# Kernel optimization log

Hardware: AMD Instinct MI355X
Metric: run time of the kernel (lower is better)

## Reference

```python
import jax, jax.numpy as jnp
from jax import lax
import numpy as np

NH = 4                      # num_heads in CrossScaleCom
KS = [3, 5, 7, 9]           # per-head depthwise kernel sizes
WS = 2                      # window_size in LocalFeatureGuided
GGM_K = 7                   # guide-token generator kernel size


def _dwconv(x, w, stride, pad):
    # depthwise conv: w has shape (C, 1, k, k), feature_group_count = C
    return lax.conv_general_dilated(
        x, w, (stride, stride), [(pad, pad), (pad, pad)],
        feature_group_count=x.shape[1],
        dimension_numbers=("NCHW", "OIHW", "NCHW"))


def _forward(x, dw_w0, dw_b0, dw_w1, dw_b1, dw_w2, dw_b2, dw_w3, dw_b3,
             csc_w, csc_b, bn_gamma, bn_beta, bn_mean, bn_var,
             ggm_w, ggm_b, qkv_w, qkv_b, proj_w, proj_b):
    B, C, H, W = x.shape
    cph = C // NH
    # ---- CrossScaleCom: per-head multi-scale depthwise convs ----
    xh = x.reshape(B, NH, cph, H, W)
    dws = [(dw_w0, dw_b0), (dw_w1, dw_b1), (dw_w2, dw_b2), (dw_w3, dw_b3)]
    heads = [_dwconv(xh[:, i], w, 1, KS[i] // 2) + b[None, :, None, None]
             for i, (w, b) in enumerate(dws)]
    y = jnp.stack(heads, 1)                      # (B, NH, cph, H, W)
    y = y.transpose(0, 2, 1, 3, 4).reshape(B, C, H, W)  # channel shuffle
    y = jnp.einsum("bchw,oc->bohw", y, csc_w) + csc_b[None, :, None, None]
    Co = y.shape[1]
    # ---- LocalFeatureGuided ----
    # ggm: BatchNorm (eval) -> GELU (exact) -> depthwise conv k=7 stride=WS
    inv = bn_gamma / jnp.sqrt(bn_var + 1e-5)
    g = (y - bn_mean[None, :, None, None]) * inv[None, :, None, None] \
        + bn_beta[None, :, None, None]
    g = jax.nn.gelu(g, approximate=False)
    g = _dwconv(g, ggm_w, WS, GGM_K // 2) + ggm_b[None, :, None, None]  # (B,Co,Ho,Wo)
    Ho, Wo = H // WS, W // WS
    L = Ho * Wo
    # unfold(kernel=WS, stride=WS) -> (B, Co, WS*WS, L), torch unfold ordering
    xu = y.reshape(B, Co, Ho, WS, Wo, WS).transpose(0, 1, 3, 5, 2, 4)
    xu = xu.reshape(B, Co, WS * WS, L)
    tokens = jnp.concatenate([g.reshape(B, Co, 1, L), xu], axis=2)  # (B,Co,5,L)
    # 1x1 conv over channel dim == einsum
    qkv = jnp.einsum("bcpl,oc->bopl", tokens, qkv_w) + qkv_b[None, :, None, None]
    q, k, v = jnp.split(qkv, 3, axis=1)          # each (B, Co, 5, L)
    # tiny 5x5 attention per (batch, channel), contracting over windows L
    attn = jnp.einsum("bcpl,bcql->bcpq", q, k) / (Co ** 0.5)
    attn = jax.nn.softmax(attn, axis=-1)
    out = jnp.einsum("bcpq,bcql->bcpl", attn, v)  # (B, Co, 5, L)
    out = out[:, :, 0, :].reshape(B, Co, Ho, Wo)  # guide-token output
    out = jnp.einsum("bchw,oc->bohw", out, proj_w) + proj_b[None, :, None, None]
    return out


def setup_inputs() -> dict:
    key = jax.random.key(0)
    ks = jax.random.split(key, 16)
    B, Cin, Cout, H, W = 8, 64, 128, 224, 224
    cph = Cin // NH
    s = 0.05
    d = {"x": jax.random.normal(ks[0], (B, Cin, H, W), jnp.float32)}
    for i, kk in enumerate(KS):
        d[f"dw_w{i}"] = jax.random.normal(ks[1 + i], (cph, 1, kk, kk), jnp.float32) * s
        d[f"dw_b{i}"] = jnp.zeros((cph,), jnp.float32)
    d["csc_w"] = jax.random.normal(ks[5], (Cout, Cin), jnp.float32) * s
    d["csc_b"] = jnp.zeros((Cout,), jnp.float32)
    d["bn_gamma"] = jnp.ones((Cout,), jnp.float32)
    d["bn_beta"] = jnp.zeros((Cout,), jnp.float32)
    d["bn_mean"] = jnp.zeros((Cout,), jnp.float32)
    d["bn_var"] = jnp.ones((Cout,), jnp.float32)
    d["ggm_w"] = jax.random.normal(ks[6], (Cout, 1, GGM_K, GGM_K), jnp.float32) * s
    d["ggm_b"] = jnp.zeros((Cout,), jnp.float32)
    d["qkv_w"] = jax.random.normal(ks[7], (3 * Cout, Cout), jnp.float32) * s
    d["qkv_b"] = jnp.zeros((3 * Cout,), jnp.float32)
    d["proj_w"] = jax.random.normal(ks[8], (Cout, Cout), jnp.float32) * s
    d["proj_b"] = jnp.zeros((Cout,), jnp.float32)
    return d


def reference(x, dw_w0, dw_b0, dw_w1, dw_b1, dw_w2, dw_b2, dw_w3, dw_b3,
              csc_w, csc_b, bn_gamma, bn_beta, bn_mean, bn_var,
              ggm_w, ggm_b, qkv_w, qkv_b, proj_w, proj_b):
    return _forward(x, dw_w0, dw_b0, dw_w1, dw_b1, dw_w2, dw_b2, dw_w3, dw_b3,
                    csc_w, csc_b, bn_gamma, bn_beta, bn_mean, bn_var,
                    ggm_w, ggm_b, qkv_w, qkv_b, proj_w, proj_b)
```

## Files before the change

### kernel.cpp

```cpp
#include <hip/hip_runtime.h>

#define BB 8
#define CIN 64
#define CO 128
#define Hdim 224
#define Wdim 224
#define HWt (224*224)
#define HO 112
#define WO 112
#define Lt (112*112)

typedef unsigned short u16;
typedef short bf16x8 __attribute__((ext_vector_type(8)));
typedef float f32x4  __attribute__((ext_vector_type(4)));
#define MFMA16(a,b,c) __builtin_amdgcn_mfma_f32_16x16x32_bf16((a),(b),(c),0,0,0)

__device__ inline u16 f2bf(float f) {
    union { float f; unsigned u; } v; v.f = f;
    unsigned r = (v.u + 0x7fffu + ((v.u >> 16) & 1u)) >> 16;
    return (u16)r;
}
__device__ inline float bf2f(u16 h) {
    union { unsigned u; float f; } v; v.u = ((unsigned)h) << 16; return v.f;
}
__device__ inline float sum8bf(uint4 v) {
    return bf2f(v.x & 0xffff) + bf2f(v.x >> 16) + bf2f(v.y & 0xffff) + bf2f(v.y >> 16)
         + bf2f(v.z & 0xffff) + bf2f(v.z >> 16) + bf2f(v.w & 0xffff) + bf2f(v.w >> 16);
}

__global__ void zero_kernel(float* __restrict__ p, int n4) {
    int i = blockIdx.x * 256 + threadIdx.x;
    if (i < n4) ((float4*)p)[i] = make_float4(0.f, 0.f, 0.f, 0.f);
}

template<int HEAD>
__global__ __launch_bounds__(256) void dw_conv(
    const float* __restrict__ x, const float* __restrict__ w,
    const float* __restrict__ bias, u16* __restrict__ dwb)
{
    constexpr int K   = 3 + 2*HEAD;
    constexpr int PAD = HEAD + 1;
    constexpr int R   = 32 + 2*PAD;
    const int tile = blockIdx.x;
    const int c    = blockIdx.y;
    const int b    = blockIdx.z;
    const int th = (tile/7)*32, tw = (tile%7)*32;
    __shared__ float patch[R*40];
    const int tid = threadIdx.x;
    const float* xin = x + (size_t)(b*CIN + HEAD*16 + c)*HWt;
    for (int idx = tid; idx < R*40; idx += 256) {
        int r = idx / 40, cc = idx - r*40;
        int gy = th - PAD + r, gx = tw - 4 + cc;
        float v = 0.f;
        if (gy >= 0 && gy < Hdim && gx >= 0 && gx < Wdim) v = xin[gy*Wdim + gx];
        patch[idx] = v;
    }
    float wreg[K*K];
    const float* wp = w + c*K*K;
    #pragma unroll
    for (int i = 0; i < K*K; i++) wreg[i] = wp[i];
    const float bv = bias[c];
    __syncthreads();

    const int ty = tid >> 3, x0 = (tid & 7) * 4;
    float acc[4] = {bv, bv, bv, bv};
    #pragma unroll
    for (int ky = 0; ky < K; ky++) {
        float rr[12];
        *(float4*)&rr[0] = *(const float4*)&patch[(ty+ky)*40 + x0];
        *(float4*)&rr[4] = *(const float4*)&patch[(ty+ky)*40 + x0 + 4];
        *(float4*)&rr[8] = *(const float4*)&patch[(ty+ky)*40 + x0 + 8];
        #pragma unroll
        for (int kx = 0; kx < K; kx++) {
            const float wv = wreg[ky*K + kx];
            #pragma unroll
            for (int j = 0; j < 4; j++)
                acc[j] = fmaf(rr[j + kx + 4 - PAD], wv, acc[j]);
        }
    }
    const int s = c*4 + HEAD;
    u16 o4[4] = {f2bf(acc[0]), f2bf(acc[1]), f2bf(acc[2]), f2bf(acc[3])};
    *(uint2*)&dwb[(size_t)(b*CIN + s)*HWt + (th+ty)*Wdim + tw + x0] = *(uint2*)o4;
}

__global__ __launch_bounds__(256) void csc_mfma(
    const float* __restrict__ W, const float* __restrict__ bias,
    const u16* __restrict__ dwb, u16* __restrict__ y4)
{
    const int b  = blockIdx.z;
    const int p0 = blockIdx.x * 128;
    __shared__ u16 Abuf[128*72];
    __shared__ u16 Tbuf[32*132];
    const int tid = threadIdx.x;
    const int wv = tid >> 6, ln = tid & 63;
    const int mh = (wv >> 1)*64, nh = (wv & 1)*64;
    const int lm = ln & 15, kq = ln >> 4;
    for (int t = tid; t < 1024; t += 256) {
        int r = t >> 3, kk = (t & 7)*8;
        const float* src = &W[r*64 + kk];
        float4 f0 = *(const float4*)src, f1 = *(const float4*)(src+4);
        u16 tmp[8] = {f2bf(f0.x),f2bf(f0.y),f2bf(f0.z),f2bf(f0.w),
                      f2bf(f1.x),f2bf(f1.y),f2bf(f1.z),f2bf(f1.w)};
        *(uint4*)&Abuf[r*72 + kk] = *(uint4*)tmp;
    }
    const u16* Db = dwb + (size_t)b*CIN*HWt;
    f32x4 acc[4][4];
    #pragma unroll
    for (int i=0;i<4;i++)
        #pragma unroll
        for (int j=0;j<4;j++) acc[i][j] = (f32x4){0.f,0.f,0.f,0.f};

    for (int kc = 0; kc < 64; kc += 32) {
        __syncthreads();
        for (int t = tid; t < 512; t += 256) {
            int k = t >> 4, n0 = (t & 15)*8;
            *(uint4*)&Tbuf[k*132 + n0] = *(const uint4*)&Db[(size_t)(kc+k)*HWt + p0 + n0];
        }
        __syncthreads();
        bf16x8 af[4], bfr[4];
        #pragma unroll
        for (int tm=0;tm<4;tm++)
            af[tm] = *(bf16x8*)&Abuf[(mh + tm*16 + lm)*72 + kc + kq*8];
        #pragma unroll
        for (int tn=0;tn<4;tn++) {
            int n = nh + tn*16 + lm;
            #pragma unroll
            for (int j=0;j<8;j++) bfr[tn][j] = (short)Tbuf[(kq*8+j)*132 + n];
        }
        #pragma unroll
        for (int tm=0;tm<4;tm++)
            #pragma unroll
            for (int tn=0;tn<4;tn++)
                acc[tm][tn] = MFMA16(af[tm], bfr[tn], acc[tm][tn]);
    }
    #pragma unroll
    for (int tm=0;tm<4;tm++) {
        #pragma unroll
        for (int r=0;r<4;r++) {
            int o = mh + tm*16 + kq*4 + r;
            float bb = bias[o];
            #pragma unroll
            for (int tn=0;tn<4;tn++) {
                int p = p0 + nh + tn*16 + lm;
                int gy = p / 224, gx = p - gy*224;
                int w = (gy&1)*2 + (gx&1);
                y4[((size_t)(b*CO + o)*4 + w)*Lt + (gy>>1)*WO + (gx>>1)]
                    = f2bf(acc[tm][tn][r] + bb);
            }
        }
    }
}

__global__ void ggm_kernel(const u16* __restrict__ y4,
    const float* __restrict__ gamma, const float* __restrict__ beta,
    const float* __restrict__ mean, const float* __restrict__ var,
    const float* __restrict__ gw, const float* __restrict__ gb,
    u16* __restrict__ gbf)
{
    const int tile = blockIdx.x;
    const int cch  = blockIdx.y;
    const int b    = blockIdx.z;
    const int ho0 = (tile/7)*16, wo0 = (tile%7)*16;
    __shared__ float patch[37*38];
    __shared__ float wl[49];
    const int tid = threadIdx.y*16+threadIdx.x;
    if (tid < 49) wl[tid] = gw[cch*49 + tid];
    const float inv = gamma[cch] * rsqrtf(var[cch] + 1e-5f);
    const float mu = mean[cch], bt = beta[cch];
    const u16* yc = y4 + (size_t)(b*CO + cch)*4*Lt;
    for (int idx = tid; idx < 37*37; idx += 256) {
        int r = idx/37, cc = idx - r*37;
        int gy = 2*ho0 - 3 + r, gx = 2*wo0 - 3 + cc;
        float v = 0.f;
        if (gy>=0 && gy<Hdim && gx>=0 && gx<Wdim) {
            int w = (gy&1)*2 + (gx&1);
            float t = (bf2f(yc[(size_t)w*Lt + (gy>>1)*WO + (gx>>1)]) - mu)*inv + bt;
            v = t * 0.5f * (1.0f + erff(t * 0.7071067811865475f));
        }
        patch[r*38+cc] = v;
    }
    __syncthreads();
    const int ty = threadIdx.y, tx = threadIdx.x;
    float acc = gb[cch];
    #pragma unroll
    for (int ky=0; ky<7; ky++)
        #pragma unroll
        for (int kx=0; kx<7; kx++)
            acc += patch[(2*ty+ky)*38 + 2*tx+kx]*wl[ky*7+kx];
    gbf[(size_t)(b*CO+cch)*Lt + (ho0+ty)*WO + (wo0+tx)] = f2bf(acc);
}

__global__ __launch_bounds__(256) void G_mfma(
    const u16* __restrict__ gbf, const u16* __restrict__ y4,
    float* __restrict__ G)
{
    const int b = blockIdx.z, p = blockIdx.y, split = blockIdx.x;
    const u16* Ab = gbf + (size_t)b*CO*Lt;
    const u16* Bb; int brs;
    if (p == 0) { Bb = Ab; brs = Lt; }
    else        { Bb = y4 + ((size_t)b*CO*4 + (p-1))*Lt; brs = 4*Lt; }
    __shared__ u16 Abuf[128*40];
    __shared__ u16 Bbuf[128*40];
    const int tid = threadIdx.x;
    const int wv = tid >> 6, ln = tid & 63;
    const int mh = (wv >> 1)*64, nh = (wv & 1)*64;
    const int lm = ln & 15, kq = ln >> 4;
    f32x4 acc[4][4];
    #pragma unroll
    for (int i=0;i<4;i++)
        #pragma unroll
        for (int j=0;j<4;j++) acc[i][j] = (f32x4){0.f,0.f,0.f,0.f};

    for (int ci = split; ci < 392; ci += 32) {
        const int l0 = ci*32;
        __syncthreads();
        for (int t = tid; t < 512; t += 256) {
            int r = t >> 2, kk = (t & 3)*8;
            *(uint4*)&Abuf[r*40 + kk] = *(const uint4*)&Ab[(size_t)r*Lt  + l0 + kk];
            *(uint4*)&Bbuf[r*40 + kk] = *(const uint4*)&Bb[(size_t)r*brs + l0 + kk];
        }
        __syncthreads();
        bf16x8 af[4], bfr[4];
        #pragma unroll
        for (int tm=0;tm<4;tm++)
            af[tm]  = *(bf16x8*)&Abuf[(mh + tm*16 + lm)*40 + kq*8];
        #pragma unroll
        for (int tn=0;tn<4;tn++)
            bfr[tn] = *(bf16x8*)&Bbuf[(nh + tn*16 + lm)*40 + kq*8];
        #pragma unroll
        for (int tm=0;tm<4;tm++)
            #pragma unroll
            for (int tn=0;tn<4;tn++)
                acc[tm][tn] = MFMA16(af[tm], bfr[tn], acc[tm][tn]);
    }
    float* Go = G + ((size_t)(b*5 + p))*CO*CO;
    #pragma unroll
    for (int tm=0;tm<4;tm++)
        #pragma unroll
        for (int r=0;r<4;r++) {
            int mrow = mh + tm*16 + kq*4 + r;
            #pragma unroll
            for (int tn=0;tn<4;tn++)
                atomicAdd(&Go[mrow*CO + nh + tn*16 + lm], acc[tm][tn][r]);
        }
}

__global__ void S_kernel(const u16* __restrict__ gbf, const u16* __restrict__ y4,
                         float* __restrict__ S)
{
    const int b = blockIdx.x >> 7, c = blockIdx.x & 127;
    const u16* gr = gbf + (size_t)(b*CO+c)*Lt;
    const u16* yr = y4  + (size_t)(b*CO+c)*4*Lt;
    float vals[5] = {0.f,0.f,0.f,0.f,0.f};
    for (int i = threadIdx.x*8; i < Lt; i += 256*8)
        vals[0] += sum8bf(*(const uint4*)&gr[i]);
    #pragma unroll
    for (int w=0; w<4; w++)
        for (int i = threadIdx.x*8; i < Lt; i += 256*8)
            vals[1+w] += sum8bf(*(const uint4*)&yr[(size_t)w*Lt + i]);
    #pragma unroll
    for (int off=32; off>0; off>>=1) {
        #pragma unroll
        for (int q=0;q<5;q++) vals[q] += __shfl_down(vals[q], off);
    }
    __shared__ float red[4][5];
    const int wid = threadIdx.x>>6, lane = threadIdx.x&63;
    if (lane==0) {
        #pragma unroll
        for (int q=0;q<5;q++) red[wid][q] = vals[q];
    }
    __syncthreads();
    if (threadIdx.x==0) {
        #pragma unroll
        for (int q=0;q<5;q++)
            S[((size_t)b*5 + q)*CO + c] = red[0][q]+red[1][q]+red[2][q]+red[3][q];
    }
}

__global__ __launch_bounds__(256) void fused_logits_kernel(
    const float* __restrict__ G, const float* __restrict__ S,
    const float* __restrict__ qkv_w, const float* __restrict__ qkv_b,
    float* __restrict__ lg)
{
    const int p = blockIdx.x, b = blockIdx.y;
    __shared__ float Wl[32*132];
    __shared__ float Al[32*132];
    __shared__ float KGl[128*128];
    const int tid = threadIdx.x;
    const int og = (tid >> 4) * 8;
    const int pg = (tid & 15) * 8;
    const float* Gp = G + (size_t)(b*5 + p)*CO*CO;
    float acc[8][8];
    #pragma unroll
    for (int i=0;i<8;i++)
        #pragma unroll
        for (int j=0;j<8;j++) acc[i][j]=0.f;

    for (int kc = 0; kc < 128; kc += 32) {
        __syncthreads();
        for (int t = tid; t < 4096; t += 256) {
            int kk = t & 31, o = t >> 5;
            Wl[kk*132 + o] = Gp[(size_t)o*CO + kc + kk];
            Al[kk*132 + o] = qkv_w[(size_t)(CO + o)*CO + kc + kk];
        }
        __syncthreads();
        #pragma unroll 4
        for (int kk = 0; kk < 32; kk++) {
            float wv[8], av[8];
            *(float4*)&wv[0] = *(const float4*)&Wl[kk*132+og];
            *(float4*)&wv[4] = *(const float4*)&Wl[kk*132+og+4];
            *(float4*)&av[0] = *(const float4*)&Al[kk*132+pg];
            *(float4*)&av[4] = *(const float4*)&Al[kk*132+pg+4];
            #pragma unroll
            for (int i=0;i<8;i++)
                #pragma unroll
                for (int j=0;j<8;j++)
                    acc[i][j] = fmaf(wv[i], av[j], acc[i][j]);
        }
    }
    #pragma unroll
    for (int i=0;i<8;i++) {
        #pragma unroll
        for (int j=0;j<8;j+=4)
            *(float4*)&KGl[(og+i)*128 + pg + j] = *(float4*)&acc[i][j];
    }
    __syncthreads();
    if (tid < 128) {
        const int c = tid;
        const float qb = qkv_b[c], kb = qkv_b[CO + c];
        const float* S0 = S + (size_t)b*5*CO;
        const float* Sp = S0 + p*CO;
        const float* qwrow = qkv_w + (size_t)c*CO;
        const float* kwrow = qkv_w + (size_t)(CO + c)*CO;
        float sq = qb * 12544.f, ks = 0.f, s = 0.f;
        for (int c2 = 0; c2 < CO; c2++) {
            sq = fmaf(qwrow[c2], S0[c2], sq);
            ks = fmaf(kwrow[c2], Sp[c2], ks);
            s  = fmaf(qwrow[c2], KGl[c2*128 + c], s);
        }
        lg[(size_t)(b*5 + p)*CO + c] = s + qb*ks + kb*sq;
    }
}

__global__ void softmax5_kernel(const float* __restrict__ lg, float* __restrict__ a)
{
    const int b = blockIdx.x, c = threadIdx.x;
    float v[5];
    #pragma unroll
    for (int p=0;p<5;p++) v[p] = lg[(size_t)(b*5 + p)*CO + c];
    const float scl = 0.08838834764831845f;
    float mx = v[0];
    #pragma unroll
    for (int p=1;p<5;p++) mx = fmaxf(mx, v[p]);
    float e[5], sum = 0.f;
    #pragma unroll
    for (int p=0;p<5;p++){ e[p] = __expf((v[p]-mx)*scl); sum += e[p]; }
    const float rs = 1.f/sum;
    #pragma unroll
    for (int p=0;p<5;p++) a[((size_t)b*CO + c)*5 + p] = e[p]*rs;
}

__global__ void F_kernel(const float* __restrict__ proj_w,
    const float* __restrict__ qkv_w, const float* __restrict__ a,
    float* __restrict__ F)
{
    const int b = blockIdx.z, p = blockIdx.y;
    const int o  = blockIdx.x*2 + (threadIdx.x>>7);
    const int cp = threadIdx.x & 127;
    const float* vw = qkv_w + 2*CO*CO;
    float s = 0.f;
    for (int c=0;c<CO;c++)
        s = fmaf(proj_w[o*CO+c] * a[((size_t)b*CO+c)*5 + p], vw[c*CO+cp], s);
    F[(((size_t)(b*5+p))*CO + o)*CO + cp] = s;
}

__global__ void bias_kernel(const float* __restrict__ proj_w,
    const float* __restrict__ proj_b, const float* __restrict__ qkv_b,
    float* __restrict__ biasout)
{
    const int o = threadIdx.x;
    const float* vb = qkv_b + 2*CO;
    float s = proj_b[o];
    for (int c=0;c<CO;c++) s = fmaf(proj_w[o*CO+c], vb[c], s);
    biasout[o] = s;
}

__global__ __launch_bounds__(256) void final_mfma(
    const float* __restrict__ F, const u16* __restrict__ gbf,
    const u16* __restrict__ y4, const float* __restrict__ biasout,
    float* __restrict__ out)
{
    const int b = blockIdx.z;
    const int p0 = blockIdx.x * 128;
    __shared__ u16 Abuf[128*40];
    __shared__ u16 Tbuf[32*132];
    const int tid = threadIdx.x;
    const int wv = tid >> 6, ln = tid & 63;
    const int mh = (wv >> 1)*64, nh = (wv & 1)*64;
    const int lm = ln & 15, kq = ln >> 4;
    f32x4 acc[4][4];
    #pragma unroll
    for (int i=0;i<4;i++)
        #pragma unroll
        for (int j=0;j<4;j++) acc[i][j] = (f32x4){0.f,0.f,0.f,0.f};

    for (int ph = 0; ph < 5; ph++) {
        const float* Fp = F + (size_t)(b*5 + ph)*CO*CO;
        const u16* Bb; int brs;
        if (ph == 0) { Bb = gbf + (size_t)b*CO*Lt; brs = Lt; }
        else         { Bb = y4 + ((size_t)b*CO*4 + (ph-1))*Lt; brs = 4*Lt; }
        for (int kc = 0; kc < CO; kc += 32) {
            __syncthreads();
            for (int t = tid; t < 512; t += 256) {
                int r = t >> 2, kk = (t & 3)*8;
                const float* src = &Fp[r*CO + kc + kk];
                float4 f0 = *(const float4*)src, f1 = *(const float4*)(src+4);
                u16 tmp[8] = {f2bf(f0.x),f2bf(f0.y),f2bf(f0.z),f2bf(f0.w),
                              f2bf(f1.x),f2bf(f1.y),f2bf(f1.z),f2bf(f1.w)};
                *(uint4*)&Abuf[r*40 + kk] = *(uint4*)tmp;
            }
            for (int t = tid; t < 512; t += 256) {
                int k = t >> 4, n0 = (t & 15)*8;
                *(uint4*)&Tbuf[k*132 + n0] = *(const uint4*)&Bb[(size_t)(kc+k)*brs + p0 + n0];
            }
            __syncthreads();
            bf16x8 af[4], bfr[4];
            #pragma unroll
            for (int tm=0;tm<4;tm++)
                af[tm] = *(bf16x8*)&Abuf[(mh + tm*16 + lm)*40 + kq*8];
            #pragma unroll
            for (int tn=0;tn<4;tn++) {
                int n = nh + tn*16 + lm;
                #pragma unroll
                for (int j=0;j<8;j++) bfr[tn][j] = (short)Tbuf[(kq*8+j)*132 + n];
            }
            #pragma unroll
            for (int tm=0;tm<4;tm++)
                #pragma unroll
                for (int tn=0;tn<4;tn++)
                    acc[tm][tn] = MFMA16(af[tm], bfr[tn], acc[tm][tn]);
        }
    }
    float* Ob = out + (size_t)b*CO*Lt;
    #pragma unroll
    for (int tm=0;tm<4;tm++) {
        #pragma unroll
        for (int r=0;r<4;r++) {
            int o = mh + tm*16 + kq*4 + r;
            float bb = biasout[o];
            #pragma unroll
            for (int tn=0;tn<4;tn++)
                Ob[(size_t)o*Lt + p0 + nh + tn*16 + lm] = acc[tm][tn][r] + bb;
        }
    }
}

extern "C" void kernel_launch(void* const* d_in, const int* in_sizes, int n_in,
                              void* d_out, int out_size, void* d_ws, size_t ws_size,
                              hipStream_t stream) {
    const float* x      = (const float*)d_in[0];
    const float* dw_w0  = (const float*)d_in[1];
    const float* dw_b0  = (const float*)d_in[2];
    const float* dw_w1  = (const float*)d_in[3];
    const float* dw_b1  = (const float*)d_in[4];
    const float* dw_w2  = (const float*)d_in[5];
    const float* dw_b2  = (const float*)d_in[6];
    const float* dw_w3  = (const float*)d_in[7];
    const float* dw_b3  = (const float*)d_in[8];
    const float* csc_w  = (const float*)d_in[9];
    const float* csc_b  = (const float*)d_in[10];
    const float* bn_g   = (const float*)d_in[11];
    const float* bn_b   = (const float*)d_in[12];
    const float* bn_m   = (const float*)d_in[13];
    const float* bn_v   = (const float*)d_in[14];
    const float* ggm_w  = (const float*)d_in[15];
    const float* ggm_b  = (const float*)d_in[16];
    const float* qkv_w  = (const float*)d_in[17];
    const float* qkv_b  = (const float*)d_in[18];
    const float* proj_w = (const float*)d_in[19];
    const float* proj_b = (const float*)d_in[20];
    float* out = (float*)d_out;

    char* ws = (char*)d_ws;
    u16*   y4  = (u16*)(ws);
    u16*   dwb = (u16*)(ws + 102760448);
    u16*   gbf = (u16*)(ws + 154140672);
    float* G   = (float*)(ws + 179830784);
    float* lgb = G  + 655360;
    float* F   = lgb + 5120;
    float* S   = F  + 655360;
    float* aw  = S  + 5120;
    float* bo  = aw + 5120;

    zero_kernel<<<dim3(640), 256, 0, stream>>>(G, 655360/4);

    dw_conv<0><<<dim3(49, 16, 8), 256, 0, stream>>>(x, dw_w0, dw_b0, dwb);
    dw_conv<1><<<dim3(49, 16, 8), 256, 0, stream>>>(x, dw_w1, dw_b1, dwb);
    dw_conv<2><<<dim3(49, 16, 8), 256, 0, stream>>>(x, dw_w2, dw_b2, dwb);
    dw_conv<3><<<dim3(49, 16, 8), 256, 0, stream>>>(x, dw_w3, dw_b3, dwb);

    csc_mfma<<<dim3(392, 1, 8), 256, 0, stream>>>(csc_w, csc_b, dwb, y4);

    ggm_kernel<<<dim3(49, 128, 8), dim3(16,16), 0, stream>>>(
        y4, bn_g, bn_b, bn_m, bn_v, ggm_w, ggm_b, gbf);

    G_mfma<<<dim3(32, 5, 8), 256, 0, stream>>>(gbf, y4, G);

    S_kernel<<<dim3(1024), 256, 0, stream>>>(gbf, y4, S);

    fused_logits_kernel<<<dim3(5, 8), 256, 0, stream>>>(G, S, qkv_w, qkv_b, lgb);

    softmax5_kernel<<<dim3(8), 128, 0, stream>>>(lgb, aw);

    F_kernel<<<dim3(64, 5, 8), 256, 0, stream>>>(proj_w, qkv_w, aw, F);
    bias_kernel<<<dim3(1), 128, 0, stream>>>(proj_w, proj_b, qkv_b, bo);

    final_mfma<<<dim3(98, 1, 8), 256, 0, stream>>>(F, gbf, y4, bo, out);
}
```

Before: 729.7 us.

## Restructure GGM depthwise conv into full-width row strips with vectorized loads

The BN+GELU+7x7 stride-2 depthwise conv kernel now has each block process a 16-output-row strip across the full width instead of a 16x16 tile. Input rows are read as 16-byte vectors and interleaved into a padded, bank-staggered shared-memory patch. Each thread computes 8 outputs with register-held weights and writes them as one vector store. Exact erf GELU is replaced by a polynomial approximation with a fast reciprocal and exp, which trades a small accuracy loss for fewer ALU cycles and less redundant halo work.

Measured after the change: 723.9 us. About the same (-0.8%).

```diff
diff --git a/kernel.cpp b/kernel.cpp
--- a/kernel.cpp
+++ b/kernel.cpp
@@ -23,9 +23,23 @@
 __device__ inline float bf2f(u16 h) {
     union { unsigned u; float f; } v; v.u = ((unsigned)h) << 16; return v.f;
 }
+__device__ inline float uasf(unsigned u) {
+    union { unsigned u; float f; } v; v.u = u; return v.f;
+}
 __device__ inline float sum8bf(uint4 v) {
     return bf2f(v.x & 0xffff) + bf2f(v.x >> 16) + bf2f(v.y & 0xffff) + bf2f(v.y >> 16)
          + bf2f(v.z & 0xffff) + bf2f(v.z >> 16) + bf2f(v.w & 0xffff) + bf2f(v.w >> 16);
+}
+
+__device__ inline float gelu_fast(float x) {
+    float z  = x * 0.7071067811865476f;
+    float az = fabsf(z);
+    float t  = __builtin_amdgcn_rcpf(fmaf(0.3275911f, az, 1.0f));
+    float p  = fmaf(fmaf(fmaf(fmaf(1.061405429f, t, -1.453152027f), t,
+                    1.421413741f), t, -0.284496736f), t, 0.254829592f);
+    float e  = __expf(-z * z);
+    float er = copysignf(1.0f - p * t * e, z);
+    return 0.5f * x * (1.0f + er);
 }
 
 __global__ void zero_kernel(float* __restrict__ p, int n4) {
@@ -151,43 +165,88 @@
     }
 }
 
-__global__ void ggm_kernel(const u16* __restrict__ y4,
+__global__ __launch_bounds__(256) void ggm_kernel(const u16* __restrict__ y4,
     const float* __restrict__ gamma, const float* __restrict__ beta,
     const float* __restrict__ mean, const float* __restrict__ var,
     const float* __restrict__ gw, const float* __restrict__ gb,
     u16* __restrict__ gbf)
 {
-    const int tile = blockIdx.x;
-    const int cch  = blockIdx.y;
-    const int b    = blockIdx.z;
-    const int ho0 = (tile/7)*16, wo0 = (tile%7)*16;
-    __shared__ float patch[37*38];
-    __shared__ float wl[49];
-    const int tid = threadIdx.y*16+threadIdx.x;
-    if (tid < 49) wl[tid] = gw[cch*49 + tid];
-    const float inv = gamma[cch] * rsqrtf(var[cch] + 1e-5f);
-    const float mu = mean[cch], bt = beta[cch];
-    const u16* yc = y4 + (size_t)(b*CO + cch)*4*Lt;
-    for (int idx = tid; idx < 37*37; idx += 256) {
-        int r = idx/37, cc = idx - r*37;
-        int gy = 2*ho0 - 3 + r, gx = 2*wo0 - 3 + cc;
-        float v = 0.f;
-        if (gy>=0 && gy<Hdim && gx>=0 && gx<Wdim) {
-            int w = (gy&1)*2 + (gx&1);
-            float t = (bf2f(yc[(size_t)w*Lt + (gy>>1)*WO + (gx>>1)]) - mu)*inv + bt;
-            v = t * 0.5f * (1.0f + erff(t * 0.7071067811865475f));
-        }
-        patch[r*38+cc] = v;
-    }
+    const int ho0 = blockIdx.x * 16;
+    const int c   = blockIdx.y;
+    const int b   = blockIdx.z;
+    __shared__ float patch[37*272];
+    const int tid = threadIdx.x;
+
+    const float inv = gamma[c] * rsqrtf(var[c] + 1e-5f);
+    const float bsh = fmaf(-mean[c], inv, beta[c]);
+    const u16* ybc = y4 + (size_t)(b*CO + c)*4*Lt;
+
+    for (int idx = tid; idx < 37*14; idx += 256) {
+        int r = idx / 14, q = idx - r*14;
+        int gy = 2*ho0 - 3 + r;
+        float* dst = &patch[r*272 + 4*((r>>1)&7) + 8 + 16*q];
+        if (gy >= 0 && gy < Hdim) {
+            const u16* pe = ybc + (size_t)((gy&1)*2)*Lt + (gy>>1)*WO + 8*q;
+            uint4 ve = *(const uint4*)pe;
+            uint4 vo = *(const uint4*)(pe + Lt);
+            unsigned eu[4] = {ve.x, ve.y, ve.z, ve.w};
+            unsigned ou[4] = {vo.x, vo.y, vo.z, vo.w};
+            float o[16];
+            #pragma unroll
+            for (int i = 0; i < 4; i++) {
+                float e0 = uasf(eu[i] << 16), e1 = uasf(eu[i] & 0xffff0000u);
+                float d0 = uasf(ou[i] << 16), d1 = uasf(ou[i] & 0xffff0000u);
+                o[4*i+0] = gelu_fast(fmaf(e0, inv, bsh));
+                o[4*i+1] = gelu_fast(fmaf(d0, inv, bsh));
+                o[4*i+2] = gelu_fast(fmaf(e1, inv, bsh));
+                o[4*i+3] = gelu_fast(fmaf(d1, inv, bsh));
+            }
+            #pragma unroll
+            for (int i = 0; i < 4; i++)
+                *(float4*)&dst[4*i] = *(float4*)&o[4*i];
+        } else {
+            float4 z = make_float4(0.f,0.f,0.f,0.f);
+            #pragma unroll
+            for (int i = 0; i < 4; i++) *(float4*)&dst[4*i] = z;
+        }
+    }
+    for (int idx = tid; idx < 37*2; idx += 256) {
+        int r = idx >> 1, side = idx & 1;
+        float* dst = &patch[r*272 + 4*((r>>1)&7) + (side ? 232 : 0)];
+        float4 z = make_float4(0.f,0.f,0.f,0.f);
+        *(float4*)&dst[0] = z; *(float4*)&dst[4] = z;
+    }
+    float wk[49];
+    const float* wp = gw + c*49;
+    #pragma unroll
+    for (int i = 0; i < 49; i++) wk[i] = wp[i];
+    const float bv = gb[c];
     __syncthreads();
-    const int ty = threadIdx.y, tx = threadIdx.x;
-    float acc = gb[cch];
-    #pragma unroll
-    for (int ky=0; ky<7; ky++)
-        #pragma unroll
-        for (int kx=0; kx<7; kx++)
-            acc += patch[(2*ty+ky)*38 + 2*tx+kx]*wl[ky*7+kx];
-    gbf[(size_t)(b*CO+cch)*Lt + (ho0+ty)*WO + (wo0+tx)] = f2bf(acc);
+
+    const int ty = tid >> 4, m = tid & 15;
+    if (m < 14) {
+        float acc[8] = {bv,bv,bv,bv,bv,bv,bv,bv};
+        #pragma unroll
+        for (int ky = 0; ky < 7; ky++) {
+            int r = 2*ty + ky;
+            const float* row = &patch[r*272 + 4*((r>>1)&7) + 16*m + 4];
+            float f[24];
+            #pragma unroll
+            for (int u = 0; u < 6; u++)
+                *(float4*)&f[4*u] = *(const float4*)&row[4*u];
+            #pragma unroll
+            for (int kx = 0; kx < 7; kx++) {
+                const float wv = wk[ky*7 + kx];
+                #pragma unroll
+                for (int j = 0; j < 8; j++)
+                    acc[j] = fmaf(f[2*j + kx + 1], wv, acc[j]);
+            }
+        }
+        u16 o8[8];
+        #pragma unroll
+        for (int j = 0; j < 8; j++) o8[j] = f2bf(acc[j]);
+        *(uint4*)&gbf[(size_t)(b*CO + c)*Lt + (ho0 + ty)*WO + 8*m] = *(uint4*)o8;
+    }
 }
 
 __global__ __launch_bounds__(256) void G_mfma(
@@ -501,7 +560,7 @@
 
     csc_mfma<<<dim3(392, 1, 8), 256, 0, stream>>>(csc_w, csc_b, dwb, y4);
 
-    ggm_kernel<<<dim3(49, 128, 8), dim3(16,16), 0, stream>>>(
+    ggm_kernel<<<dim3(7, 128, 8), 256, 0, stream>>>(
         y4, bn_g, bn_b, bn_m, bn_v, ggm_w, ggm_b, gbf);
 
     G_mfma<<<dim3(32, 5, 8), 256, 0, stream>>>(gbf, y4, G);
```
